# Performance work log

Measured on AMD Instinct MI355X. Metric: run time of the kernel, lower is better.

The kernel has to match this reference:

```python
import jax, jax.numpy as jnp
import numpy as np

NUM_GROUPS = 32
NUM_HEADS = 8
EPS = 1e-6


def group_norm(x, gamma, beta):
    B, C, H, W = x.shape
    xg = x.reshape(B, NUM_GROUPS, C // NUM_GROUPS, H, W)
    mean = xg.mean(axis=(2, 3, 4), keepdims=True)
    var = xg.var(axis=(2, 3, 4), keepdims=True)
    xn = (xg - mean) * jax.lax.rsqrt(var + EPS)
    xn = xn.reshape(B, C, H, W)
    return xn * gamma[None, :, None, None] + beta[None, :, None, None]


def setup_inputs() -> dict:
    key = jax.random.key(0)
    ks = jax.random.split(key, 3)
    B, C, H, W = 8, 512, 32, 32
    x = jax.random.normal(ks[0], (B, C, H, W), dtype=jnp.float32)
    # xavier_uniform for conv1x1: fan_in=C, fan_out per weight
    lim_qkv = float(np.sqrt(6.0 / (C + 3 * C)))
    w_qkv = jax.random.uniform(ks[1], (3 * C, C), minval=-lim_qkv, maxval=lim_qkv, dtype=jnp.float32)
    b_qkv = jnp.zeros((3 * C,), dtype=jnp.float32)
    lim_p = float(np.sqrt(6.0 / (C + C)))
    w_proj = jax.random.uniform(ks[2], (C, C), minval=-lim_p, maxval=lim_p, dtype=jnp.float32)
    b_proj = jnp.zeros((C,), dtype=jnp.float32)
    gamma = jnp.ones((C,), dtype=jnp.float32)
    beta = jnp.zeros((C,), dtype=jnp.float32)
    return {"x": x, "gamma": gamma, "beta": beta, "w_qkv": w_qkv, "b_qkv": b_qkv,
            "w_proj": w_proj, "b_proj": b_proj}


def reference(x, gamma, beta, w_qkv, b_qkv, w_proj, b_proj):
    B, C, H, W = x.shape
    N = H * W
    hd = C // NUM_HEADS
    scale = hd ** -0.5

    x_norm = group_norm(x, gamma, beta)
    # conv1x1 == channel GEMM: (B,C,H,W) -> (B,3C,H,W)
    qkv = jnp.einsum('bchw,oc->bohw', x_norm, w_qkv) + b_qkv[None, :, None, None]
    qkv = qkv.reshape(B, 3, NUM_HEADS, hd, N).transpose(1, 0, 2, 4, 3)
    q, k, v = qkv[0], qkv[1], qkv[2]

    attn = jnp.einsum('bhnd,bhmd->bhnm', q, k) * scale
    attn = jax.nn.softmax(attn, axis=-1)
    out = jnp.einsum('bhnm,bhmd->bhnd', attn, v)

    out = out.transpose(0, 1, 3, 2).reshape(B, C, H, W)
    out = jnp.einsum('bchw,oc->bohw', out, w_proj) + b_proj[None, :, None, None]
    return x + out
```

## Files before the change

### kernel.cpp

```cpp
#include <hip/hip_runtime.h>

#define LOG2E 1.4426950408889634f

typedef short bf16x8 __attribute__((ext_vector_type(8)));
typedef short short4v __attribute__((ext_vector_type(4)));
typedef float f32x4 __attribute__((ext_vector_type(4)));
typedef _Float16 half4v __attribute__((ext_vector_type(4)));
typedef unsigned u32x4 __attribute__((ext_vector_type(4)));
typedef unsigned __attribute__((address_space(1))) u32g;
typedef unsigned __attribute__((address_space(3))) u32l;

#define MFMA16(a, b, c) __builtin_amdgcn_mfma_f32_16x16x32_bf16((a), (b), (c), 0, 0, 0)

__device__ __forceinline__ short f2bf(float f) {
  unsigned u = __builtin_bit_cast(unsigned, f);
  u += 0x7FFFu + ((u >> 16) & 1u);
  return (short)(u >> 16);
}

__device__ __forceinline__ unsigned cvtpk(float lo, float hi) {
  unsigned r;
  asm("v_cvt_pk_bf16_f32 %0, %1, %2" : "=v"(r) : "v"(lo), "v"(hi));
  return r;
}

__device__ __forceinline__ void g2l16(void* lds, const void* g) {
  __builtin_amdgcn_global_load_lds((u32g*)const_cast<void*>(g), (u32l*)lds, 16, 0, 0);
}

__global__ __launch_bounds__(256) void gn_kernel(const float* __restrict__ x,
                                                 const float* __restrict__ gamma,
                                                 const float* __restrict__ beta,
                                                 short* __restrict__ xn_t) {
  __shared__ _Float16 xs[16 * 1024];
  __shared__ float red[8];
  const int bg = blockIdx.x;
  const int b = bg >> 5, g = bg & 31;
  const int t = threadIdx.x;
  const float4* gx4 = (const float4*)(x + (size_t)(b * 512 + g * 16) * 1024);
  float s1 = 0.f, s2 = 0.f;
  for (int i = 0; i < 16; ++i) {
    float4 v = gx4[t + 256 * i];
    s1 += (v.x + v.y) + (v.z + v.w);
    s2 += (v.x * v.x + v.y * v.y) + (v.z * v.z + v.w * v.w);
    half4v pk = {(_Float16)v.x, (_Float16)v.y, (_Float16)v.z, (_Float16)v.w};
    *(half4v*)((char*)xs + i * 2048 + ((8 * t) ^ ((i & 7) << 4))) = pk;
  }
  for (int m = 1; m < 64; m <<= 1) {
    s1 += __shfl_xor(s1, m);
    s2 += __shfl_xor(s2, m);
  }
  if ((t & 63) == 0) {
    red[(t >> 6) * 2] = s1;
    red[(t >> 6) * 2 + 1] = s2;
  }
  __syncthreads();
  s1 = (red[0] + red[2]) + (red[4] + red[6]);
  s2 = (red[1] + red[3]) + (red[5] + red[7]);
  const float mean = s1 * (1.f / 16384.f);
  const float var = s2 * (1.f / 16384.f) - mean * mean;
  const float rstd = rsqrtf(var + 1e-6f);
  const int ci = t & 15;
  const float ga = gamma[g * 16 + ci] * rstd;
  const float be = beta[g * 16 + ci] - mean * ga;
  short* dst = xn_t + (size_t)b * 1024 * 512 + g * 16 + ci;
  const int sw = (ci & 7) << 4;
  for (int i = 0; i < 64; ++i) {
    int n = (t >> 4) + 16 * i;
    float v = (float)*(const _Float16*)((const char*)xs + ci * 2048 + ((2 * n) ^ sw));
    dst[(size_t)n * 512] = f2bf(fmaf(v, ga, be));
  }
}

__global__ __launch_bounds__(256) void f2bf_kernel(const float* __restrict__ src,
                                                   short* __restrict__ dst, int n4) {
  int i = blockIdx.x * 256 + threadIdx.x;
  if (i < n4) {
    float4 v = ((const float4*)src)[i];
    short4v o = {f2bf(v.x), f2bf(v.y), f2bf(v.z), f2bf(v.w)};
    *(short4v*)(dst + (size_t)i * 4) = o;
  }
}

__global__ __launch_bounds__(256) void qkv_gemm(const short* __restrict__ W,
                                                const short* __restrict__ xn,
                                                const float* __restrict__ bias,
                                                short* __restrict__ qbuf,
                                                short* __restrict__ kbuf,
                                                short* __restrict__ vtbuf) {
  __shared__ short a_sm[2][128 * 32];
  __shared__ short b_sm[2][128 * 32];
  const int t = threadIdx.x;
  const int lane = t & 63, w = t >> 6;
  const int nbase = blockIdx.x * 128;
  const int mbase = blockIdx.y * 128;
  const int b = blockIdx.z;
  const short* Asrc = W + (size_t)mbase * 512;
  const short* Bsrc = xn + (size_t)b * 1024 * 512 + (size_t)nbase * 512;

  const int j0 = t, j1 = t + 256;
  const int r0 = j0 >> 2, c0 = ((j0 & 3) ^ ((j0 >> 3) & 3)) * 8;
  const int r1 = j1 >> 2, c1 = ((j1 & 3) ^ ((j1 >> 3) & 3)) * 8;

#define STAGE(bi, kt)                                                 \
  {                                                                   \
    const int k0s = (kt) * 32;                                        \
    g2l16(&a_sm[bi][j0 * 8], Asrc + (size_t)r0 * 512 + k0s + c0);     \
    g2l16(&a_sm[bi][j1 * 8], Asrc + (size_t)r1 * 512 + k0s + c1);     \
    g2l16(&b_sm[bi][j0 * 8], Bsrc + (size_t)r0 * 512 + k0s + c0);     \
    g2l16(&b_sm[bi][j1 * 8], Bsrc + (size_t)r1 * 512 + k0s + c1);     \
  }

  const int wm = (w >> 1) * 64, wn = (w & 1) * 64;
  const int col = lane & 15, rg = lane >> 4;

  f32x4 acc[4][4] = {};

  STAGE(0, 0)
  __syncthreads();
  int cur = 0;

  for (int kt = 0; kt < 16; ++kt) {
    if (kt < 15) STAGE(cur ^ 1, kt + 1);
    bf16x8 af[4], bfr[4];
#pragma unroll
    for (int mf = 0; mf < 4; ++mf) {
      const int row = wm + mf * 16 + col;
      af[mf] = *(const bf16x8*)&a_sm[cur][row * 32 + ((rg ^ ((row >> 1) & 3)) * 8)];
    }
#pragma unroll
    for (int nf = 0; nf < 4; ++nf) {
      const int row = wn + nf * 16 + col;
      bfr[nf] = *(const bf16x8*)&b_sm[cur][row * 32 + ((rg ^ ((row >> 1) & 3)) * 8)];
    }
    __builtin_amdgcn_s_setprio(1);
#pragma unroll
    for (int mf = 0; mf < 4; ++mf)
#pragma unroll
      for (int nf = 0; nf < 4; ++nf)
        acc[mf][nf] = MFMA16(af[mf], bfr[nf], acc[mf][nf]);
    __builtin_amdgcn_s_setprio(0);
    __syncthreads();
    cur ^= 1;
  }
#undef STAGE

  const int section = mbase >> 9;
  for (int mf = 0; mf < 4; ++mf) {
    const int o0 = mbase + wm + mf * 16 + rg * 4;
    const int h = (o0 >> 6) & 7, d0 = o0 & 63;
    float b4[4];
    for (int r = 0; r < 4; ++r) b4[r] = bias[o0 + r];
    for (int nf = 0; nf < 4; ++nf) {
      const int n = nbase + wn + nf * 16 + col;
      if (section < 2) {
        short4v pkv;
        for (int r = 0; r < 4; ++r) pkv[r] = f2bf(acc[mf][nf][r] + b4[r]);
        short* dst = (section == 0) ? qbuf : kbuf;
        *(short4v*)&dst[((size_t)(b * 8 + h) * 1024 + n) * 64 + d0] = pkv;
      } else {
        for (int r = 0; r < 4; ++r)
          vtbuf[((size_t)(b * 8 + h) * 64 + d0 + r) * 1024 + n] =
              f2bf(acc[mf][nf][r] + b4[r]);
      }
    }
  }
}

__global__ __launch_bounds__(256, 2) void attn_kernel(const short* __restrict__ qbuf,
                                                      const short* __restrict__ kbuf,
                                                      const short* __restrict__ vtbuf,
                                                      short* __restrict__ ao) {
  __shared__ short k_sm[3][64 * 64];
  __shared__ short v_sm[3][64 * 64];
  const int t = threadIdx.x, lane = t & 63, w = t >> 6;
  const int col = lane & 15, rg = lane >> 4;
  const int bh = blockIdx.x, qt = blockIdx.y;
  const int b = bh >> 3, h = bh & 7;
  const int qbase = qt * 128 + w * 32;

  bf16x8 aq[2][2];
  {
    const short* qp = qbuf + ((size_t)bh * 1024 + qbase) * 64;
#pragma unroll
    for (int mf = 0; mf < 2; ++mf)
#pragma unroll
      for (int kc = 0; kc < 2; ++kc)
        aq[mf][kc] = *(const bf16x8*)&qp[(mf * 16 + col) * 64 + kc * 32 + rg * 8];
  }

  const short* kp0 = kbuf + (size_t)bh * 65536;
  const short* vp0 = vtbuf + (size_t)bh * 65536;

  uint4 kr[2], vr[2];
#define LOADK(kt)                                                                  \
  _Pragma("unroll") for (int i = 0; i < 2; ++i) {                                  \
    int j = t + 256 * i;                                                           \
    kr[i] = *(const uint4*)&kp0[((size_t)(kt)*64 + (j >> 3)) * 64 + (j & 7) * 8];  \
  }
#define LOADV(kt)                                                                  \
  _Pragma("unroll") for (int i = 0; i < 2; ++i) {                                  \
    int j = t + 256 * i;                                                           \
    vr[i] = *(const uint4*)&vp0[(size_t)(j >> 3) * 1024 + (kt)*64 + (j & 7) * 8];  \
  }
#define WRITEKP(dst)                                                               \
  _Pragma("unroll") for (int i = 0; i < 2; ++i) {                                  \
    int j = t + 256 * i;                                                           \
    int row = j >> 3, off = j & 7;                                                 \
    *(uint4*)((char*)(dst) + row * 128 + ((off * 16) ^ ((row & 7) << 4))) = kr[i]; \
  }
#define WRITEVP(dst)                                                               \
  _Pragma("unroll") for (int i = 0; i < 2; ++i) {                                  \
    int j = t + 256 * i;                                                           \
    int d = j >> 3, g = j & 7;                                                     \
    int base = (g >> 2) * 64 + (g & 1) * 32 + ((g >> 1) & 1) * 8;                  \
    char* vb = (char*)(dst) + d * 128;                                             \
    uint2 lo = {vr[i].x, vr[i].y}, hi = {vr[i].z, vr[i].w};                        \
    *(uint2*)(vb + ((base) ^ ((d & 7) << 4))) = lo;                                \
    *(uint2*)(vb + ((base + 16) ^ ((d & 7) << 4))) = hi;                           \
  }

#define QKB(sT, kptr)                                                   \
  __builtin_amdgcn_s_setprio(1);                                        \
  _Pragma("unroll") for (int nf = 0; nf < 4; ++nf) {                    \
    const int n = nf * 16 + col;                                        \
    const char* kb = (const char*)(kptr) + n * 128;                     \
    const int sw = (n & 7) << 4;                                        \
    bf16x8 bk0 = *(const bf16x8*)(kb + ((rg * 16) ^ sw));               \
    bf16x8 bk1 = *(const bf16x8*)(kb + ((64 + rg * 16) ^ sw));          \
    _Pragma("unroll") for (int mf = 0; mf < 2; ++mf) {                  \
      f32x4 z = {};                                                     \
      z = MFMA16(bk0, aq[mf][0], z);                                    \
      sT[mf][nf] = MFMA16(bk1, aq[mf][1], z);                           \
    }                                                                   \
  }                                                                     \
  __builtin_amdgcn_s_setprio(0);

#define SMB(sT)                                                             \
  _Pragma("unroll") for (int mf = 0; mf < 2; ++mf) {                        \
    f32x4 mv = sT[mf][0];                                                   \
    _Pragma("unroll") for (int nf = 1; nf < 4; ++nf)                        \
        _Pragma("unroll") for (int r = 0; r < 4; ++r)                       \
            mv[r] = fmaxf(mv[r], sT[mf][nf][r]);                            \
    float mx = fmaxf(fmaxf(mv[0], mv[1]), fmaxf(mv[2], mv[3]));             \
    mx = fmaxf(mx, __shfl_xor(mx, 16));                                     \
    mx = fmaxf(mx, __shfl_xor(mx, 32));                                     \
    const float pmax = mx * 0.125f;                                         \
    if (!__all(pmax <= mrun[mf] + 8.f)) {                                   \
      const float mnew = fmaxf(mrun[mf], pmax);                             \
      const float alpha = __builtin_amdgcn_exp2f((mrun[mf] - mnew) * LOG2E);\
      mrun[mf] = mnew;                                                      \
      lrun[mf] *= alpha;                                                    \
      _Pragma("unroll") for (int df = 0; df < 4; ++df) oacc[mf][df] *= alpha; \
    }                                                                       \
    const float nege = mrun[mf] * LOG2E;                                    \
    float psum = 0.f;                                                       \
    _Pragma("unroll") for (int nf = 0; nf < 4; ++nf) {                      \
      float p0 = __builtin_amdgcn_exp2f(fmaf(sT[mf][nf][0], kSL2E, -nege)); \
      float p1 = __builtin_amdgcn_exp2f(fmaf(sT[mf][nf][1], kSL2E, -nege)); \
      float p2 = __builtin_amdgcn_exp2f(fmaf(sT[mf][nf][2], kSL2E, -nege)); \
      float p3 = __builtin_amdgcn_exp2f(fmaf(sT[mf][nf][3], kSL2E, -nege)); \
      psum += (p0 + p1) + (p2 + p3);                                        \
      pk[mf][nf][0] = cvtpk(p0, p1);                                        \
      pk[mf][nf][1] = cvtpk(p2, p3);                                        \
    }                                                                       \
    psum += __shfl_xor(psum, 16);                                           \
    psum += __shfl_xor(psum, 32);                                           \
    lrun[mf] += psum;                                                       \
  }

#define PVB(vptr)                                                           \
  __builtin_amdgcn_s_setprio(1);                                            \
  _Pragma("unroll") for (int kc = 0; kc < 2; ++kc) {                        \
    bf16x8 pb[2];                                                           \
    _Pragma("unroll") for (int mf = 0; mf < 2; ++mf) {                      \
      u32x4 pbu = {pk[mf][2 * kc][0], pk[mf][2 * kc][1],                    \
                   pk[mf][2 * kc + 1][0], pk[mf][2 * kc + 1][1]};           \
      pb[mf] = __builtin_bit_cast(bf16x8, pbu);                             \
    }                                                                       \
    _Pragma("unroll") for (int df = 0; df < 4; ++df) {                      \
      const int d = df * 16 + col;                                          \
      bf16x8 av = *(const bf16x8*)((const char*)(vptr) + d * 128 +          \
                                   ((kc * 64 + rg * 16) ^ ((d & 7) << 4))); \
      _Pragma("unroll") for (int mf = 0; mf < 2; ++mf)                      \
          oacc[mf][df] = MFMA16(av, pb[mf], oacc[mf][df]);                  \
    }                                                                       \
  }                                                                         \
  __builtin_amdgcn_s_setprio(0);

#define ITER(kt, sTc, sTn)                                                  \
  {                                                                         \
    if ((kt) + 2 < 16) { LOADK((kt) + 2) LOADV((kt) + 2) }                  \
    if ((kt) + 1 < 16) { QKB(sTn, kQ) }                                     \
    SMB(sTc)                                                                \
    PVB(vP)                                                                 \
    if ((kt) + 2 < 16) { WRITEKP(kW) WRITEVP(vW) }                          \
    __syncthreads();                                                        \
    short* tk = kP; kP = kQ; kQ = kW; kW = tk;                              \
    short* tv = vP; vP = vQ; vQ = vW; vW = tv;                              \
  }

  f32x4 oacc[2][4] = {};
  float mrun[2] = {-3e38f, -3e38f}, lrun[2] = {0.f, 0.f};
  const float kSL2E = 0.125f * LOG2E;
  unsigned pk[2][4][2];
  f32x4 sA[2][4], sB[2][4];

  short *kP = k_sm[0], *kQ = k_sm[1], *kW = k_sm[2];
  short *vP = v_sm[0], *vQ = v_sm[1], *vW = v_sm[2];

  LOADK(0) LOADV(0)
  WRITEKP(kP) WRITEVP(vP)
  LOADK(1) LOADV(1)
  __syncthreads();
  QKB(sA, kP)
  WRITEKP(kQ) WRITEVP(vQ)
  __syncthreads();

  for (int kt2 = 0; kt2 < 16; kt2 += 2) {
    ITER(kt2, sA, sB)
    ITER(kt2 + 1, sB, sA)
  }

#pragma unroll
  for (int mf = 0; mf < 2; ++mf) {
    const float rl = 1.f / lrun[mf];
    const int q = qbase + mf * 16 + col;
    short* dst = ao + ((size_t)b * 1024 + q) * 512 + h * 64;
#pragma unroll
    for (int df = 0; df < 4; ++df) {
      short4v pkv;
#pragma unroll
      for (int r = 0; r < 4; ++r) pkv[r] = f2bf(oacc[mf][df][r] * rl);
      *(short4v*)&dst[df * 16 + rg * 4] = pkv;
    }
  }
#undef LOADK
#undef LOADV
#undef WRITEKP
#undef WRITEVP
#undef QKB
#undef SMB
#undef PVB
#undef ITER
}

__global__ __launch_bounds__(256) void proj_gemm(const short* __restrict__ W,
                                                 const short* __restrict__ ao,
                                                 const float* __restrict__ bias,
                                                 const float* __restrict__ x,
                                                 float* __restrict__ out) {
  __shared__ short a_sm[2][64 * 32];
  __shared__ short b_sm[2][128 * 32];
  const int t = threadIdx.x;
  const int lane = t & 63, w = t >> 6;
  const int nbase = blockIdx.x * 128;
  const int mbase = blockIdx.y * 64;
  const int b = blockIdx.z;
  const short* Asrc = W + (size_t)mbase * 512;
  const short* Bsrc = ao + (size_t)b * 1024 * 512 + (size_t)nbase * 512;

  const int j0 = t, j1 = t + 256;
  const int r0 = j0 >> 2, c0 = ((j0 & 3) ^ ((j0 >> 3) & 3)) * 8;
  const int r1 = j1 >> 2, c1 = ((j1 & 3) ^ ((j1 >> 3) & 3)) * 8;

#define STAGE(bi, kt)                                                 \
  {                                                                   \
    const int k0s = (kt) * 32;                                        \
    g2l16(&a_sm[bi][j0 * 8], Asrc + (size_t)r0 * 512 + k0s + c0);     \
    g2l16(&b_sm[bi][j0 * 8], Bsrc + (size_t)r0 * 512 + k0s + c0);     \
    g2l16(&b_sm[bi][j1 * 8], Bsrc + (size_t)r1 * 512 + k0s + c1);     \
  }

  const int wm = (w >> 1) * 32, wn = (w & 1) * 64;
  const int col = lane & 15, rg = lane >> 4;

  f32x4 acc[2][4] = {};

  STAGE(0, 0)
  __syncthreads();
  int cur = 0;

  for (int kt = 0; kt < 16; ++kt) {
    if (kt < 15) STAGE(cur ^ 1, kt + 1);
    bf16x8 af[2], bfr[4];
#pragma unroll
    for (int mf = 0; mf < 2; ++mf) {
      const int row = wm + mf * 16 + col;
      af[mf] = *(const bf16x8*)&a_sm[cur][row * 32 + ((rg ^ ((row >> 1) & 3)) * 8)];
    }
#pragma unroll
    for (int nf = 0; nf < 4; ++nf) {
      const int row = wn + nf * 16 + col;
      bfr[nf] = *(const bf16x8*)&b_sm[cur][row * 32 + ((rg ^ ((row >> 1) & 3)) * 8)];
    }
    __builtin_amdgcn_s_setprio(1);
#pragma unroll
    for (int mf = 0; mf < 2; ++mf)
#pragma unroll
      for (int nf = 0; nf < 4; ++nf)
        acc[mf][nf] = MFMA16(af[mf], bfr[nf], acc[mf][nf]);
    __builtin_amdgcn_s_setprio(0);
    __syncthreads();
    cur ^= 1;
  }
#undef STAGE

  for (int mf = 0; mf < 2; ++mf) {
    const int o0 = mbase + wm + mf * 16 + rg * 4;
    float b4[4];
    for (int r = 0; r < 4; ++r) b4[r] = bias[o0 + r];
    for (int nf = 0; nf < 4; ++nf) {
      const int n = nbase + wn + nf * 16 + col;
      for (int r = 0; r < 4; ++r) {
        size_t idx = ((size_t)b * 512 + o0 + r) * 1024 + n;
        out[idx] = x[idx] + acc[mf][nf][r] + b4[r];
      }
    }
  }
}

extern "C" void kernel_launch(void* const* d_in, const int* in_sizes, int n_in,
                              void* d_out, int out_size, void* d_ws, size_t ws_size,
                              hipStream_t stream) {
  const float* x = (const float*)d_in[0];
  const float* gamma = (const float*)d_in[1];
  const float* beta = (const float*)d_in[2];
  const float* w_qkv = (const float*)d_in[3];
  const float* b_qkv = (const float*)d_in[4];
  const float* w_proj = (const float*)d_in[5];
  const float* b_proj = (const float*)d_in[6];
  float* out = (float*)d_out;

  char* ws = (char*)d_ws;
  short* xn_t = (short*)(ws);
  short* wqkv_b = (short*)(ws + 8388608);
  short* wproj_b = (short*)(ws + 9961472);
  short* qbuf = (short*)(ws + 10485760);
  short* kbuf = (short*)(ws + 18874368);
  short* vtbuf = (short*)(ws + 27262976);
  short* aobuf = (short*)(ws + 35651584);

  gn_kernel<<<dim3(256), dim3(256), 0, stream>>>(x, gamma, beta, xn_t);
  f2bf_kernel<<<dim3(768), dim3(256), 0, stream>>>(w_qkv, wqkv_b, 196608);
  f2bf_kernel<<<dim3(256), dim3(256), 0, stream>>>(w_proj, wproj_b, 65536);
  qkv_gemm<<<dim3(8, 12, 8), dim3(256), 0, stream>>>(wqkv_b, xn_t, b_qkv, qbuf, kbuf,
                                                     vtbuf);
  attn_kernel<<<dim3(64, 8), dim3(256), 0, stream>>>(qbuf, kbuf, vtbuf, aobuf);
  proj_gemm<<<dim3(8, 8, 8), dim3(256), 0, stream>>>(wproj_b, aobuf, b_proj, x, out);
}
```

Before: 86.76 us.

## Load K/V fragments straight from global into registers in attention kernel

Removes the shared-memory triple buffering of K and V tiles in the attention kernel. Each wave now loads its MFMA operand fragments directly from global memory into registers, double-buffering K in registers and loading V right before use. This drops the LDS writes/reads and the __syncthreads per tile. In exchange, each of the four waves separately fetches the same K/V data, relying on the cache, and V loads are narrow 8-byte reads with little latency hiding.

After: 139.4 us. 1.61x slower.

```diff
diff --git a/kernel.cpp b/kernel.cpp
--- a/kernel.cpp
+++ b/kernel.cpp
@@ -171,8 +171,6 @@
                                                       const short* __restrict__ kbuf,
                                                       const short* __restrict__ vtbuf,
                                                       short* __restrict__ ao) {
-  __shared__ short k_sm[3][64 * 64];
-  __shared__ short v_sm[3][64 * 64];
   const int t = threadIdx.x, lane = t & 63, w = t >> 6;
   const int col = lane & 15, rg = lane >> 4;
   const int bh = blockIdx.x, qt = blockIdx.y;
@@ -189,54 +187,35 @@
         aq[mf][kc] = *(const bf16x8*)&qp[(mf * 16 + col) * 64 + kc * 32 + rg * 8];
   }
 
-  const short* kp0 = kbuf + (size_t)bh * 65536;
-  const short* vp0 = vtbuf + (size_t)bh * 65536;
-
-  uint4 kr[2], vr[2];
-#define LOADK(kt)                                                                  \
-  _Pragma("unroll") for (int i = 0; i < 2; ++i) {                                  \
-    int j = t + 256 * i;                                                           \
-    kr[i] = *(const uint4*)&kp0[((size_t)(kt)*64 + (j >> 3)) * 64 + (j & 7) * 8];  \
-  }
-#define LOADV(kt)                                                                  \
-  _Pragma("unroll") for (int i = 0; i < 2; ++i) {                                  \
-    int j = t + 256 * i;                                                           \
-    vr[i] = *(const uint4*)&vp0[(size_t)(j >> 3) * 1024 + (kt)*64 + (j & 7) * 8];  \
-  }
-#define WRITEKP(dst)                                                               \
-  _Pragma("unroll") for (int i = 0; i < 2; ++i) {                                  \
-    int j = t + 256 * i;                                                           \
-    int row = j >> 3, off = j & 7;                                                 \
-    *(uint4*)((char*)(dst) + row * 128 + ((off * 16) ^ ((row & 7) << 4))) = kr[i]; \
-  }
-#define WRITEVP(dst)                                                               \
-  _Pragma("unroll") for (int i = 0; i < 2; ++i) {                                  \
-    int j = t + 256 * i;                                                           \
-    int d = j >> 3, g = j & 7;                                                     \
-    int base = (g >> 2) * 64 + (g & 1) * 32 + ((g >> 1) & 1) * 8;                  \
-    char* vb = (char*)(dst) + d * 128;                                             \
-    uint2 lo = {vr[i].x, vr[i].y}, hi = {vr[i].z, vr[i].w};                        \
-    *(uint2*)(vb + ((base) ^ ((d & 7) << 4))) = lo;                                \
-    *(uint2*)(vb + ((base + 16) ^ ((d & 7) << 4))) = hi;                           \
-  }
-
-#define QKB(sT, kptr)                                                   \
-  __builtin_amdgcn_s_setprio(1);                                        \
-  _Pragma("unroll") for (int nf = 0; nf < 4; ++nf) {                    \
-    const int n = nf * 16 + col;                                        \
-    const char* kb = (const char*)(kptr) + n * 128;                     \
-    const int sw = (n & 7) << 4;                                        \
-    bf16x8 bk0 = *(const bf16x8*)(kb + ((rg * 16) ^ sw));               \
-    bf16x8 bk1 = *(const bf16x8*)(kb + ((64 + rg * 16) ^ sw));          \
-    _Pragma("unroll") for (int mf = 0; mf < 2; ++mf) {                  \
-      f32x4 z = {};                                                     \
-      z = MFMA16(bk0, aq[mf][0], z);                                    \
-      sT[mf][nf] = MFMA16(bk1, aq[mf][1], z);                           \
-    }                                                                   \
-  }                                                                     \
+  const short* kl = kbuf + (size_t)bh * 65536 + col * 64 + rg * 8;
+  const short* vl = vtbuf + (size_t)bh * 65536 + col * 1024 + rg * 4;
+
+  bf16x8 kA[4][2], kB[4][2];
+  uint2 vv[2][4][2];
+
+#define LOADKM(dst, kt)                                               \
+  _Pragma("unroll") for (int nf = 0; nf < 4; ++nf)                    \
+      _Pragma("unroll") for (int c = 0; c < 2; ++c)                   \
+          dst[nf][c] = *(const bf16x8*)&kl[(kt)*4096 + nf * 1024 + c * 32];
+
+#define LOADVM(kt)                                                    \
+  _Pragma("unroll") for (int kc = 0; kc < 2; ++kc)                    \
+      _Pragma("unroll") for (int df = 0; df < 4; ++df) {              \
+    vv[kc][df][0] = *(const uint2*)&vl[df * 16384 + (kt)*64 + kc * 32];      \
+    vv[kc][df][1] = *(const uint2*)&vl[df * 16384 + (kt)*64 + kc * 32 + 16]; \
+  }
+
+#define QKM(ka)                                                       \
+  __builtin_amdgcn_s_setprio(1);                                      \
+  _Pragma("unroll") for (int nf = 0; nf < 4; ++nf)                    \
+      _Pragma("unroll") for (int mf = 0; mf < 2; ++mf) {              \
+    f32x4 z = {};                                                     \
+    z = MFMA16(ka[nf][0], aq[mf][0], z);                              \
+    sT[mf][nf] = MFMA16(ka[nf][1], aq[mf][1], z);                     \
+  }                                                                   \
   __builtin_amdgcn_s_setprio(0);
 
-#define SMB(sT)                                                             \
+#define SMB()                                                               \
   _Pragma("unroll") for (int mf = 0; mf < 2; ++mf) {                        \
     f32x4 mv = sT[mf][0];                                                   \
     _Pragma("unroll") for (int nf = 1; nf < 4; ++nf)                        \
@@ -269,7 +248,7 @@
     lrun[mf] += psum;                                                       \
   }
 
-#define PVB(vptr)                                                           \
+#define PVM()                                                               \
   __builtin_amdgcn_s_setprio(1);                                            \
   _Pragma("unroll") for (int kc = 0; kc < 2; ++kc) {                        \
     bf16x8 pb[2];                                                           \
@@ -279,47 +258,33 @@
       pb[mf] = __builtin_bit_cast(bf16x8, pbu);                             \
     }                                                                       \
     _Pragma("unroll") for (int df = 0; df < 4; ++df) {                      \
-      const int d = df * 16 + col;                                          \
-      bf16x8 av = *(const bf16x8*)((const char*)(vptr) + d * 128 +          \
-                                   ((kc * 64 + rg * 16) ^ ((d & 7) << 4))); \
+      u32x4 avu = {vv[kc][df][0].x, vv[kc][df][0].y,                        \
+                   vv[kc][df][1].x, vv[kc][df][1].y};                       \
+      bf16x8 av = __builtin_bit_cast(bf16x8, avu);                          \
       _Pragma("unroll") for (int mf = 0; mf < 2; ++mf)                      \
           oacc[mf][df] = MFMA16(av, pb[mf], oacc[mf][df]);                  \
     }                                                                       \
   }                                                                         \
   __builtin_amdgcn_s_setprio(0);
 
-#define ITER(kt, sTc, sTn)                                                  \
-  {                                                                         \
-    if ((kt) + 2 < 16) { LOADK((kt) + 2) LOADV((kt) + 2) }                  \
-    if ((kt) + 1 < 16) { QKB(sTn, kQ) }                                     \
-    SMB(sTc)                                                                \
-    PVB(vP)                                                                 \
-    if ((kt) + 2 < 16) { WRITEKP(kW) WRITEVP(vW) }                          \
-    __syncthreads();                                                        \
-    short* tk = kP; kP = kQ; kQ = kW; kW = tk;                              \
-    short* tv = vP; vP = vQ; vQ = vW; vW = tv;                              \
-  }
-
   f32x4 oacc[2][4] = {};
+  f32x4 sT[2][4];
   float mrun[2] = {-3e38f, -3e38f}, lrun[2] = {0.f, 0.f};
   const float kSL2E = 0.125f * LOG2E;
   unsigned pk[2][4][2];
-  f32x4 sA[2][4], sB[2][4];
-
-  short *kP = k_sm[0], *kQ = k_sm[1], *kW = k_sm[2];
-  short *vP = v_sm[0], *vQ = v_sm[1], *vW = v_sm[2];
-
-  LOADK(0) LOADV(0)
-  WRITEKP(kP) WRITEVP(vP)
-  LOADK(1) LOADV(1)
-  __syncthreads();
-  QKB(sA, kP)
-  WRITEKP(kQ) WRITEVP(vQ)
-  __syncthreads();
-
+
+  LOADKM(kA, 0)
   for (int kt2 = 0; kt2 < 16; kt2 += 2) {
-    ITER(kt2, sA, sB)
-    ITER(kt2 + 1, sB, sA)
+    LOADKM(kB, kt2 + 1)
+    LOADVM(kt2)
+    QKM(kA)
+    SMB()
+    PVM()
+    if (kt2 < 14) LOADKM(kA, kt2 + 2)
+    LOADVM(kt2 + 1)
+    QKM(kB)
+    SMB()
+    PVM()
   }
 
 #pragma unroll
@@ -335,14 +300,11 @@
       *(short4v*)&dst[df * 16 + rg * 4] = pkv;
     }
   }
-#undef LOADK
-#undef LOADV
-#undef WRITEKP
-#undef WRITEVP
-#undef QKB
+#undef LOADKM
+#undef LOADVM
+#undef QKM
 #undef SMB
-#undef PVB
-#undef ITER
+#undef PVM
 }
 
 __global__ __launch_bounds__(256) void proj_gemm(const short* __restrict__ W,
```
